# Kernel tuning notes

Hardware: AMD Instinct MI355X
Metric: run time of the kernel (lower is better)

The kernel has to match this reference:

```python
import jax, jax.numpy as jnp
import numpy as np

DIM = 1024
N_HEADS = 16


def setup_inputs() -> dict:
    key = jax.random.key(0)
    ks = jax.random.split(key, 9)
    B, S, D = 4, 2048, DIM
    inp = {
        "q": jax.random.normal(ks[0], (B, S, D), dtype=jnp.float32),
        "k": jax.random.normal(ks[1], (B, S, D), dtype=jnp.float32),
        "v": jax.random.normal(ks[2], (B, S, D), dtype=jnp.float32),
        "mask": jnp.ones((B, S), dtype=jnp.float32),
        # nn.Linear params for q, k, v projections (weight: [out,in], bias: [out])
        "wq": jax.random.normal(ks[3], (D, D), dtype=jnp.float32) / np.sqrt(D),
        "bq": jnp.zeros((D,), dtype=jnp.float32),
        "wk": jax.random.normal(ks[4], (D, D), dtype=jnp.float32) / np.sqrt(D),
        "bk": jnp.zeros((D,), dtype=jnp.float32),
        "wv": jax.random.normal(ks[5], (D, D), dtype=jnp.float32) / np.sqrt(D),
        "bv": jnp.zeros((D,), dtype=jnp.float32),
    }
    return inp


def reference(q, k, v, mask, wq, bq, wk, bk, wv, bv):
    B, Sq, D = q.shape
    Skv = k.shape[1]
    H = N_HEADS
    Dh = D // H
    # QKV projections (nn.Linear: x @ W^T + b)
    qp = q @ wq.T + bq
    kp = k @ wk.T + bk
    vp = v @ wv.T + bv
    # split heads: (B, S, H, Dh) -> (B, H, S, Dh)
    qh = qp.reshape(B, Sq, H, Dh).transpose(0, 2, 1, 3)
    kh = kp.reshape(B, Skv, H, Dh).transpose(0, 2, 1, 3)
    vh = vp.reshape(B, Skv, H, Dh).transpose(0, 2, 1, 3)
    # scores: (B, H, Sq, Skv)
    scores = jnp.einsum("bhqd,bhkd->bhqk", qh, kh) / np.sqrt(Dh).astype(np.float32)
    # additive mask (mask is (B, kv_len) -> (B, 1, 1, kv_len))
    scores = scores - 10000.0 * (1.0 - mask[:, None, None, :])
    attn = jax.nn.softmax(scores, axis=-1)
    out = jnp.einsum("bhqk,bhkd->bhqd", attn, vh)
    # merge heads: (B, Sq, D)
    out = out.transpose(0, 2, 1, 3).reshape(B, Sq, D)
    return out
```

## Files before the change

### kernel.cpp

```cpp
#include <hip/hip_runtime.h>
#include <hip/hip_bf16.h>
#include <stdint.h>

typedef __attribute__((ext_vector_type(4))) float f32x4;
typedef __attribute__((ext_vector_type(16))) float f32x16;
typedef __attribute__((ext_vector_type(8))) short bf16x8;

#define AS1 __attribute__((address_space(1)))
#define AS3 __attribute__((address_space(3)))

#if defined(__has_builtin)
#if __has_builtin(__builtin_amdgcn_exp2f)
#define EXPF(x) __builtin_amdgcn_exp2f(x)
#define UNITS 1.4426950408889634f
#endif
#endif
#ifndef EXPF
#define EXPF(x) __expf(x)
#define UNITS 1.0f
#endif

static __device__ __forceinline__ unsigned short f2bf(float f) {
  union { float f; unsigned u; } v; v.f = f;
  unsigned r = v.u + 0x7fffu + ((v.u >> 16) & 1u);
  return (unsigned short)(r >> 16);
}

static __device__ __forceinline__ unsigned pkbf(float lo, float hi) {
  __hip_bfloat162 h2 = __float22bfloat162_rn(make_float2(lo, hi));
  union { __hip_bfloat162 h; unsigned u; } c; c.h = h2; return c.u;
}

__global__ __launch_bounds__(256) void conv_all(
    const float* __restrict__ q, const float* __restrict__ k, const float* __restrict__ v,
    const float* __restrict__ wq, const float* __restrict__ wk, const float* __restrict__ wv,
    unsigned short* __restrict__ Xq, unsigned short* __restrict__ Xk, unsigned short* __restrict__ Xv,
    unsigned short* __restrict__ Wq, unsigned short* __restrict__ Wk, unsigned short* __restrict__ Wv) {
  int bid = blockIdx.x;
  const float* src; unsigned short* dst; int base;
  if (bid < 12288) {
    int t = bid >> 12;
    base = (bid & 4095) * 2048;
    if (t == 0) { src = q; dst = Xq; }
    else if (t == 1) { src = k; dst = Xk; }
    else { src = v; dst = Xv; }
  } else {
    int r = bid - 12288;
    int t = r >> 9;
    base = (r & 511) * 2048;
    if (t == 0) { src = wq; dst = Wq; }
    else if (t == 1) { src = wk; dst = Wk; }
    else { src = wv; dst = Wv; }
  }
  int i = base + threadIdx.x * 8;
  float4 x0 = *(const float4*)(src + i);
  float4 x1 = *(const float4*)(src + i + 4);
  ushort4 o0, o1;
  o0.x = f2bf(x0.x); o0.y = f2bf(x0.y); o0.z = f2bf(x0.z); o0.w = f2bf(x0.w);
  o1.x = f2bf(x1.x); o1.y = f2bf(x1.y); o1.z = f2bf(x1.z); o1.w = f2bf(x1.w);
  *(ushort4*)(dst + i) = o0;
  *(ushort4*)(dst + i + 4) = o1;
}

__global__ __launch_bounds__(256) void proj_gemm3(
    const unsigned short* __restrict__ Xq, const unsigned short* __restrict__ Xk,
    const unsigned short* __restrict__ Xv,
    const unsigned short* __restrict__ Wqp, const unsigned short* __restrict__ Wkp,
    const unsigned short* __restrict__ Wvp,
    const float* __restrict__ bq, const float* __restrict__ bk, const float* __restrict__ bv,
    unsigned short* __restrict__ Qh, unsigned short* __restrict__ Kh,
    unsigned short* __restrict__ Vt) {
  const int K = 1024, S = 2048, H = 16;
  int z = blockIdx.z;
  const unsigned short *A, *W; const float* bias; unsigned short* dst; int transpose_v;
  if (z == 0)      { A = Xq; W = Wqp; bias = bq; dst = Qh; transpose_v = 0; }
  else if (z == 1) { A = Xk; W = Wkp; bias = bk; dst = Kh; transpose_v = 0; }
  else             { A = Xv; W = Wvp; bias = bv; dst = Vt; transpose_v = 1; }

  __shared__ unsigned short As[2][128 * 32];
  __shared__ unsigned short Bs[2][128 * 32];
  const int tid = threadIdx.x;
  const int l = tid & 63;
  const int w = tid >> 6;
  const int m0 = blockIdx.x * 128, n0 = blockIdx.y * 128;
  const int wm = w >> 1, wn = w & 1;

  f32x4 acc[4][4] = {};

  const int srow = (l >> 2);
  const int skc = (l & 3) * 8;

#define STAGE(buf, k0)                                                            \
  {                                                                               \
    _Pragma("unroll")                                                             \
    for (int i = 0; i < 2; ++i) {                                                 \
      int slot = w * 2 + i;                                                       \
      int row = slot * 16 + srow;                                                 \
      const unsigned short* ga = A + (long)(m0 + row) * K + (k0) + skc;           \
      const unsigned short* gb = W + (long)(n0 + row) * K + (k0) + skc;           \
      __builtin_amdgcn_global_load_lds((const AS1 unsigned int*)ga,               \
                                       (AS3 unsigned int*)(As[buf] + slot * 512 + l * 8), \
                                       16, 0, 0);                                 \
      __builtin_amdgcn_global_load_lds((const AS1 unsigned int*)gb,               \
                                       (AS3 unsigned int*)(Bs[buf] + slot * 512 + l * 8), \
                                       16, 0, 0);                                 \
    }                                                                             \
  }

  STAGE(0, 0);
  __syncthreads();

  int cur = 0;
  for (int k0 = 0; k0 < K; k0 += 32) {
    if (k0 + 32 < K) STAGE(cur ^ 1, k0 + 32);

    bf16x8 af[4], bfr[4];
    const int kc = (l >> 4) * 8;
#pragma unroll
    for (int mi = 0; mi < 4; ++mi)
      af[mi] = *(const bf16x8*)&As[cur][(wm * 64 + mi * 16 + (l & 15)) * 32 + kc];
#pragma unroll
    for (int ni = 0; ni < 4; ++ni)
      bfr[ni] = *(const bf16x8*)&Bs[cur][(wn * 64 + ni * 16 + (l & 15)) * 32 + kc];
#pragma unroll
    for (int mi = 0; mi < 4; ++mi)
#pragma unroll
      for (int ni = 0; ni < 4; ++ni)
        acc[mi][ni] = __builtin_amdgcn_mfma_f32_16x16x32_bf16(af[mi], bfr[ni], acc[mi][ni], 0, 0, 0);

    __syncthreads();
    cur ^= 1;
  }
#undef STAGE

#pragma unroll
  for (int ni = 0; ni < 4; ++ni) {
    int col = n0 + wn * 64 + ni * 16 + (l & 15);
    float bv_ = bias[col];
    int h = col >> 6, dh = col & 63;
#pragma unroll
    for (int mi = 0; mi < 4; ++mi) {
#pragma unroll
      for (int r = 0; r < 4; ++r) {
        int m = m0 + wm * 64 + mi * 16 + (l >> 4) * 4 + r;
        int b = m >> 11, s = m & 2047;
        unsigned short obf = f2bf(acc[mi][ni][r] + bv_);
        long addr;
        if (!transpose_v)
          addr = ((long)(b * H + h) * S + s) * 64 + dh;
        else
          addr = ((long)(b * H + h) * 64 + dh) * S + s;
        dst[addr] = obf;
      }
    }
  }
}

__device__ __forceinline__ void stage_tile(const unsigned short* __restrict__ kb,
                                           const unsigned short* __restrict__ vb,
                                           char* Kb, char* Vb, int kv0, int tid) {
#pragma unroll
  for (int j = 0; j < 2; ++j) {
    int c = tid + j * 256;
    int r = c >> 3;
    int s = (c & 7) ^ (r & 7);
    const unsigned short* gk = kb + (kv0 + r) * 64 + s * 8;
    const unsigned short* gv = vb + r * 2048 + kv0 + s * 8;
    __builtin_amdgcn_global_load_lds((const AS1 unsigned int*)gk,
                                     (AS3 unsigned int*)(Kb + c * 16), 16, 0, 0);
    __builtin_amdgcn_global_load_lds((const AS1 unsigned int*)gv,
                                     (AS3 unsigned int*)(Vb + c * 16), 16, 0, 0);
  }
}

__device__ __forceinline__ void compute_tile(const char* Kb, const char* Vb,
                                             const bf16x8 (&qf)[4],
                                             const float* __restrict__ mask_b,
                                             int kv0, int hi, int qc,
                                             f32x16 (&acco)[2], float& m_run, float& lrow) {
  const float kSc = 0.125f * UNITS;
  const float THR = 8.0f * UNITS;
  const float MC = 10000.0f * UNITS;
  const int kx = qc & 7;

  bf16x8 kf[2][4], vf[2][4];
#pragma unroll
  for (int ks = 0; ks < 2; ++ks)
#pragma unroll
    for (int dc = 0; dc < 4; ++dc)
      kf[ks][dc] = *(const bf16x8*)(Kb + (ks * 32 + qc) * 128 + (((dc * 2 + hi) ^ kx) * 16));
#pragma unroll
  for (int dt = 0; dt < 2; ++dt)
#pragma unroll
    for (int c2 = 0; c2 < 4; ++c2)
      vf[dt][c2] = *(const bf16x8*)(Vb + (dt * 32 + qc) * 128 + (((c2 * 2 + hi) ^ kx) * 16));

  f32x16 st0 = {}, st1 = {};
  __builtin_amdgcn_s_setprio(1);
#pragma unroll
  for (int dc = 0; dc < 4; ++dc) {
    st0 = __builtin_amdgcn_mfma_f32_32x32x16_bf16(kf[0][dc], qf[dc], st0, 0, 0, 0);
    st1 = __builtin_amdgcn_mfma_f32_32x32x16_bf16(kf[1][dc], qf[dc], st1, 0, 0, 0);
  }
  __builtin_amdgcn_s_setprio(0);

  float mf[2][16];
#pragma unroll
  for (int ks = 0; ks < 2; ++ks)
#pragma unroll
    for (int g = 0; g < 4; ++g) {
      float4 t = *(const float4*)&mask_b[kv0 + ks * 32 + 4 * hi + g * 8];
      mf[ks][g * 4 + 0] = fmaf(t.x, MC, -MC); mf[ks][g * 4 + 1] = fmaf(t.y, MC, -MC);
      mf[ks][g * 4 + 2] = fmaf(t.z, MC, -MC); mf[ks][g * 4 + 3] = fmaf(t.w, MC, -MC);
    }
  float p[2][16];
#pragma unroll
  for (int r = 0; r < 16; ++r) {
    p[0][r] = fmaf(st0[r], kSc, mf[0][r]);
    p[1][r] = fmaf(st1[r], kSc, mf[1][r]);
  }

  float a0 = p[0][0], a1 = p[0][1], a2 = p[0][2], a3 = p[0][3];
#pragma unroll
  for (int r = 4; r < 16; r += 4) {
    a0 = fmaxf(a0, p[0][r]); a1 = fmaxf(a1, p[0][r + 1]);
    a2 = fmaxf(a2, p[0][r + 2]); a3 = fmaxf(a3, p[0][r + 3]);
  }
#pragma unroll
  for (int r = 0; r < 16; r += 4) {
    a0 = fmaxf(a0, p[1][r]); a1 = fmaxf(a1, p[1][r + 1]);
    a2 = fmaxf(a2, p[1][r + 2]); a3 = fmaxf(a3, p[1][r + 3]);
  }
  float pm = fmaxf(fmaxf(a0, a1), fmaxf(a2, a3));
  pm = fmaxf(pm, __shfl_xor(pm, 32));

  if (!__all(pm <= m_run + THR)) {
    float mnew = fmaxf(m_run, pm);
    float scl = EXPF(m_run - mnew);
    lrow *= scl;
#pragma unroll
    for (int dt = 0; dt < 2; ++dt)
#pragma unroll
      for (int r = 0; r < 16; ++r) acco[dt][r] *= scl;
    m_run = mnew;
  }

  float s0 = 0.f, s1 = 0.f, s2 = 0.f, s3 = 0.f;
#pragma unroll
  for (int ks = 0; ks < 2; ++ks)
#pragma unroll
    for (int r = 0; r < 16; r += 4) {
      p[ks][r]     = EXPF(p[ks][r] - m_run);     s0 += p[ks][r];
      p[ks][r + 1] = EXPF(p[ks][r + 1] - m_run); s1 += p[ks][r + 1];
      p[ks][r + 2] = EXPF(p[ks][r + 2] - m_run); s2 += p[ks][r + 2];
      p[ks][r + 3] = EXPF(p[ks][r + 3] - m_run); s3 += p[ks][r + 3];
    }
  float ps = (s0 + s1) + (s2 + s3);
  ps += __shfl_xor(ps, 32);
  lrow += ps;

#pragma unroll
  for (int ks = 0; ks < 2; ++ks) {
    unsigned cp0 = pkbf(p[ks][0], p[ks][1]);
    unsigned cp1 = pkbf(p[ks][2], p[ks][3]);
    unsigned cp2 = pkbf(p[ks][4], p[ks][5]);
    unsigned cp3 = pkbf(p[ks][6], p[ks][7]);
    unsigned cp4 = pkbf(p[ks][8], p[ks][9]);
    unsigned cp5 = pkbf(p[ks][10], p[ks][11]);
    unsigned cp6 = pkbf(p[ks][12], p[ks][13]);
    unsigned cp7 = pkbf(p[ks][14], p[ks][15]);
    asm volatile("v_permlane32_swap_b32 %0, %1" : "+v"(cp0), "+v"(cp2));
    asm volatile("v_permlane32_swap_b32 %0, %1" : "+v"(cp1), "+v"(cp3));
    asm volatile("v_permlane32_swap_b32 %0, %1" : "+v"(cp4), "+v"(cp6));
    asm volatile("v_permlane32_swap_b32 %0, %1" : "+v"(cp5), "+v"(cp7));
    union { unsigned u[4]; bf16x8 v; } B0, B1;
    B0.u[0] = cp0; B0.u[1] = cp1; B0.u[2] = cp2; B0.u[3] = cp3;
    B1.u[0] = cp4; B1.u[1] = cp5; B1.u[2] = cp6; B1.u[3] = cp7;
    __builtin_amdgcn_s_setprio(1);
    acco[0] = __builtin_amdgcn_mfma_f32_32x32x16_bf16(vf[0][ks * 2 + 0], B0.v, acco[0], 0, 0, 0);
    acco[1] = __builtin_amdgcn_mfma_f32_32x32x16_bf16(vf[1][ks * 2 + 0], B0.v, acco[1], 0, 0, 0);
    acco[0] = __builtin_amdgcn_mfma_f32_32x32x16_bf16(vf[0][ks * 2 + 1], B1.v, acco[0], 0, 0, 0);
    acco[1] = __builtin_amdgcn_mfma_f32_32x32x16_bf16(vf[1][ks * 2 + 1], B1.v, acco[1], 0, 0, 0);
    __builtin_amdgcn_s_setprio(0);
  }
}

__global__ __launch_bounds__(256) void attn_kernel(const unsigned short* __restrict__ qh,
                                                   const unsigned short* __restrict__ kh,
                                                   const unsigned short* __restrict__ vt,
                                                   const float* __restrict__ mask,
                                                   float* __restrict__ out) {
  const int S = 2048;
  int bid = blockIdx.x;
  int xcd = bid & 7, jj = bid >> 3;
  int bh = xcd * 8 + (jj & 7);
  int qblk = jj >> 3;
  int b = bh >> 4, h = bh & 15;
  int tid = threadIdx.x, l = tid & 63, w = tid >> 6;
  int hi = l >> 5, qc = l & 31;

  const unsigned short* qb = qh + (long)bh * S * 64;
  const unsigned short* kb = kh + (long)bh * S * 64;
  const unsigned short* vb = vt + (long)bh * 64 * S;
  const float* mask_b = mask + (long)b * S;

  __shared__ __align__(16) char pool[32768];

  const int q0 = qblk * 128 + w * 32;

  bf16x8 qf[4];
#pragma unroll
  for (int dc = 0; dc < 4; ++dc)
    qf[dc] = *(const bf16x8*)&qb[(q0 + qc) * 64 + dc * 16 + 8 * hi];

  f32x16 acco[2] = {};
  float m_run = -1e30f, lrow = 0.0f;

  stage_tile(kb, vb, pool, pool + 8192, 0, tid);
  __syncthreads();

  for (int t = 0; t < 32; ++t) {
    char* cur = pool + (t & 1) * 16384;
    if (t < 31) {
      char* nxt = pool + ((t + 1) & 1) * 16384;
      stage_tile(kb, vb, nxt, nxt + 8192, (t + 1) * 64, tid);
    }
    compute_tile(cur, cur + 8192, qf, mask_b, t * 64, hi, qc, acco, m_run, lrow);
    __syncthreads();
  }

  float (*olds)[16][65] = (float (*)[16][65])pool;
  float linv = 1.0f / lrow;
#pragma unroll
  for (int pass = 0; pass < 2; ++pass) {
    if ((qc >> 4) == pass) {
#pragma unroll
      for (int dt = 0; dt < 2; ++dt)
#pragma unroll
        for (int r = 0; r < 16; ++r) {
          int d = dt * 32 + (r & 3) + 8 * (r >> 2) + 4 * hi;
          olds[w][qc & 15][d] = acco[dt][r] * linv;
        }
    }
    asm volatile("s_waitcnt lgkmcnt(0)" ::: "memory");
#pragma unroll
    for (int r = 0; r < 16; ++r) {
      float val = olds[w][r][l];
      out[((long)b * 2048 + q0 + pass * 16 + r) * 1024 + h * 64 + l] = val;
    }
    asm volatile("s_waitcnt lgkmcnt(0)" ::: "memory");
  }
}

extern "C" void kernel_launch(void* const* d_in, const int* in_sizes, int n_in,
                              void* d_out, int out_size, void* d_ws, size_t ws_size,
                              hipStream_t stream) {
  const float* q  = (const float*)d_in[0];
  const float* k  = (const float*)d_in[1];
  const float* v  = (const float*)d_in[2];
  const float* mask = (const float*)d_in[3];
  const float* wq = (const float*)d_in[4];
  const float* bq = (const float*)d_in[5];
  const float* wk = (const float*)d_in[6];
  const float* bk = (const float*)d_in[7];
  const float* wv = (const float*)d_in[8];
  const float* bv = (const float*)d_in[9];
  float* out = (float*)d_out;

  char* ws = (char*)d_ws;
  unsigned short* Xq = (unsigned short*)(ws);
  unsigned short* Xk = (unsigned short*)(ws + 16777216L);
  unsigned short* Xv = (unsigned short*)(ws + 33554432L);
  unsigned short* Wq = (unsigned short*)(ws + 50331648L);
  unsigned short* Wk = (unsigned short*)(ws + 52428800L);
  unsigned short* Wv = (unsigned short*)(ws + 54525952L);
  unsigned short* Qh = (unsigned short*)(ws + 56623104L);
  unsigned short* Kh = (unsigned short*)(ws + 73400320L);
  unsigned short* Vt = (unsigned short*)(ws + 90177536L);

  conv_all<<<13824, 256, 0, stream>>>(q, k, v, wq, wk, wv, Xq, Xk, Xv, Wq, Wk, Wv);

  dim3 ggrid(64, 8, 3);
  proj_gemm3<<<ggrid, 256, 0, stream>>>(Xq, Xk, Xv, Wq, Wk, Wv, bq, bk, bv, Qh, Kh, Vt);

  attn_kernel<<<1024, 256, 0, stream>>>(Qh, Kh, Vt, mask, out);
}
```

Before: 377.3 us.

## Use 8 waves in projection GEMM and precompute mask bias in LDS

The projection GEMM now launches 512 threads per block with 8 waves in a 2x4 layout. Each wave owns a 64x32 output tile, and each thread stages one 16-byte chunk per operand, which halves per-thread loads and accumulators. This is meant to raise occupancy and latency hiding, at the cost of lower per-wave operand reuse. Separately, the attention kernel precomputes the additive mask bias into a 2048-float shared array once per block, so the per-tile global mask loads and FMAs go away. The price is 8KB more LDS per block. The mask preload is not followed by a barrier before its first use, though the barrier after the first stage_tile covers it.

```diff
diff --git a/kernel.cpp b/kernel.cpp
--- a/kernel.cpp
+++ b/kernel.cpp
@@ -62,7 +62,7 @@
   *(ushort4*)(dst + i + 4) = o1;
 }
 
-__global__ __launch_bounds__(256) void proj_gemm3(
+__global__ __launch_bounds__(512) void proj_gemm3(
     const unsigned short* __restrict__ Xq, const unsigned short* __restrict__ Xk,
     const unsigned short* __restrict__ Xv,
     const unsigned short* __restrict__ Wqp, const unsigned short* __restrict__ Wkp,
@@ -83,28 +83,23 @@
   const int l = tid & 63;
   const int w = tid >> 6;
   const int m0 = blockIdx.x * 128, n0 = blockIdx.y * 128;
-  const int wm = w >> 1, wn = w & 1;
-
-  f32x4 acc[4][4] = {};
-
-  const int srow = (l >> 2);
-  const int skc = (l & 3) * 8;
+  const int wm = w >> 2, wn = w & 3;
+
+  f32x4 acc[4][2] = {};
+
+  const int srow = tid >> 2;
+  const int scol = (tid & 3) * 8;
 
 #define STAGE(buf, k0)                                                            \
   {                                                                               \
-    _Pragma("unroll")                                                             \
-    for (int i = 0; i < 2; ++i) {                                                 \
-      int slot = w * 2 + i;                                                       \
-      int row = slot * 16 + srow;                                                 \
-      const unsigned short* ga = A + (long)(m0 + row) * K + (k0) + skc;           \
-      const unsigned short* gb = W + (long)(n0 + row) * K + (k0) + skc;           \
-      __builtin_amdgcn_global_load_lds((const AS1 unsigned int*)ga,               \
-                                       (AS3 unsigned int*)(As[buf] + slot * 512 + l * 8), \
-                                       16, 0, 0);                                 \
-      __builtin_amdgcn_global_load_lds((const AS1 unsigned int*)gb,               \
-                                       (AS3 unsigned int*)(Bs[buf] + slot * 512 + l * 8), \
-                                       16, 0, 0);                                 \
-    }                                                                             \
+    const unsigned short* ga = A + (long)(m0 + srow) * K + (k0) + scol;           \
+    const unsigned short* gb = W + (long)(n0 + srow) * K + (k0) + scol;           \
+    __builtin_amdgcn_global_load_lds((const AS1 unsigned int*)ga,                 \
+                                     (AS3 unsigned int*)(As[buf] + tid * 8),      \
+                                     16, 0, 0);                                   \
+    __builtin_amdgcn_global_load_lds((const AS1 unsigned int*)gb,                 \
+                                     (AS3 unsigned int*)(Bs[buf] + tid * 8),      \
+                                     16, 0, 0);                                   \
   }
 
   STAGE(0, 0);
@@ -114,18 +109,18 @@
   for (int k0 = 0; k0 < K; k0 += 32) {
     if (k0 + 32 < K) STAGE(cur ^ 1, k0 + 32);
 
-    bf16x8 af[4], bfr[4];
+    bf16x8 af[4], bfr[2];
     const int kc = (l >> 4) * 8;
 #pragma unroll
     for (int mi = 0; mi < 4; ++mi)
       af[mi] = *(const bf16x8*)&As[cur][(wm * 64 + mi * 16 + (l & 15)) * 32 + kc];
 #pragma unroll
-    for (int ni = 0; ni < 4; ++ni)
-      bfr[ni] = *(const bf16x8*)&Bs[cur][(wn * 64 + ni * 16 + (l & 15)) * 32 + kc];
+    for (int ni = 0; ni < 2; ++ni)
+      bfr[ni] = *(const bf16x8*)&Bs[cur][(wn * 32 + ni * 16 + (l & 15)) * 32 + kc];
 #pragma unroll
     for (int mi = 0; mi < 4; ++mi)
 #pragma unroll
-      for (int ni = 0; ni < 4; ++ni)
+      for (int ni = 0; ni < 2; ++ni)
         acc[mi][ni] = __builtin_amdgcn_mfma_f32_16x16x32_bf16(af[mi], bfr[ni], acc[mi][ni], 0, 0, 0);
 
     __syncthreads();
@@ -134,8 +129,8 @@
 #undef STAGE
 
 #pragma unroll
-  for (int ni = 0; ni < 4; ++ni) {
-    int col = n0 + wn * 64 + ni * 16 + (l & 15);
+  for (int ni = 0; ni < 2; ++ni) {
+    int col = n0 + wn * 32 + ni * 16 + (l & 15);
     float bv_ = bias[col];
     int h = col >> 6, dh = col & 63;
 #pragma unroll
@@ -175,12 +170,11 @@
 
 __device__ __forceinline__ void compute_tile(const char* Kb, const char* Vb,
                                              const bf16x8 (&qf)[4],
-                                             const float* __restrict__ mask_b,
+                                             const float* __restrict__ smask,
                                              int kv0, int hi, int qc,
                                              f32x16 (&acco)[2], float& m_run, float& lrow) {
   const float kSc = 0.125f * UNITS;
   const float THR = 8.0f * UNITS;
-  const float MC = 10000.0f * UNITS;
   const int kx = qc & 7;
 
   bf16x8 kf[2][4], vf[2][4];
@@ -209,9 +203,9 @@
   for (int ks = 0; ks < 2; ++ks)
 #pragma unroll
     for (int g = 0; g < 4; ++g) {
-      float4 t = *(const float4*)&mask_b[kv0 + ks * 32 + 4 * hi + g * 8];
-      mf[ks][g * 4 + 0] = fmaf(t.x, MC, -MC); mf[ks][g * 4 + 1] = fmaf(t.y, MC, -MC);
-      mf[ks][g * 4 + 2] = fmaf(t.z, MC, -MC); mf[ks][g * 4 + 3] = fmaf(t.w, MC, -MC);
+      float4 t = *(const float4*)&smask[kv0 + ks * 32 + 4 * hi + g * 8];
+      mf[ks][g * 4 + 0] = t.x; mf[ks][g * 4 + 1] = t.y;
+      mf[ks][g * 4 + 2] = t.z; mf[ks][g * 4 + 3] = t.w;
     }
   float p[2][16];
 #pragma unroll
@@ -302,9 +296,11 @@
   const unsigned short* qb = qh + (long)bh * S * 64;
   const unsigned short* kb = kh + (long)bh * S * 64;
   const unsigned short* vb = vt + (long)bh * 64 * S;
-  const float* mask_b = mask + (long)b * S;
-
+
+  __shared__ float smask[2048];
   __shared__ __align__(16) char pool[32768];
+  for (int i = tid; i < S; i += 256)
+    smask[i] = (-10000.0f * UNITS) * (1.0f - mask[b * S + i]);
 
   const int q0 = qblk * 128 + w * 32;
 
@@ -325,7 +321,7 @@
       char* nxt = pool + ((t + 1) & 1) * 16384;
       stage_tile(kb, vb, nxt, nxt + 8192, (t + 1) * 64, tid);
     }
-    compute_tile(cur, cur + 8192, qf, mask_b, t * 64, hi, qc, acco, m_run, lrow);
+    compute_tile(cur, cur + 8192, qf, smask, t * 64, hi, qc, acco, m_run, lrow);
     __syncthreads();
   }
 
@@ -381,7 +377,7 @@
   conv_all<<<13824, 256, 0, stream>>>(q, k, v, wq, wk, wv, Xq, Xk, Xv, Wq, Wk, Wv);
 
   dim3 ggrid(64, 8, 3);
-  proj_gemm3<<<ggrid, 256, 0, stream>>>(Xq, Xk, Xv, Wq, Wk, Wv, bq, bk, bv, Qh, Kh, Vt);
+  proj_gemm3<<<ggrid, 512, 0, stream>>>(Xq, Xk, Xv, Wq, Wk, Wv, bq, bk, bv, Qh, Kh, Vt);
 
   attn_kernel<<<1024, 256, 0, stream>>>(Qh, Kh, Vt, mask, out);
 }
```

After: 356.9 us. 5.4% less time.
